# Kernel tuning notes

Hardware: AMD Instinct MI355X
Metric: run time of the kernel (lower is better)

## Reference

```python
import jax, jax.numpy as jnp
import numpy as np

L, H, DIN, T, B = 3, 512, 512, 256, 64


def _lstm_layer(x, m, h0, c0, Wih, Whh, b, reverse):
    # x: [T,B,Din], m: [T,B,1], h0/c0: [B,H], Wih: [4H,Din], Whh: [4H,H], b: [4H]
    def step(carry, xm):
        h, c = carry
        xt, mt = xm
        gates = xt @ Wih.T + h @ Whh.T + b  # [B,4H]
        i, f, g, o = jnp.split(gates, 4, axis=-1)
        c_n = (jax.nn.sigmoid(f) * c + jax.nn.sigmoid(i) * jnp.tanh(g)) * mt
        h_n = jax.nn.sigmoid(o) * jnp.tanh(c_n) * mt
        return (h_n, c_n), h_n
    (hT, cT), hs = jax.lax.scan(step, (h0, c0), (x, m), reverse=reverse)
    return hs, hT, cT


def setup_inputs():
    key = jax.random.key(0)
    ks = jax.random.split(key, 16)
    s = 0.05
    return {
        "x": jax.random.normal(ks[0], (T, B, DIN), jnp.float32),
        "masks": (jax.random.uniform(ks[1], (T, B, 1)) < 0.9).astype(jnp.float32),
        "f_Wih0": jax.random.normal(ks[2], (4 * H, DIN), jnp.float32) * s,
        "f_Wih_rest": jax.random.normal(ks[3], (L - 1, 4 * H, 2 * H), jnp.float32) * s,
        "f_Whh": jax.random.normal(ks[4], (L, 4 * H, H), jnp.float32) * s,
        "f_b": jnp.zeros((L, 4 * H), jnp.float32),
        "b_Wih0": jax.random.normal(ks[5], (4 * H, DIN), jnp.float32) * s,
        "b_Wih_rest": jax.random.normal(ks[6], (L - 1, 4 * H, 2 * H), jnp.float32) * s,
        "b_Whh": jax.random.normal(ks[7], (L, 4 * H, H), jnp.float32) * s,
        "b_b": jnp.zeros((L, 4 * H), jnp.float32),
        "f_init": jax.random.normal(ks[8], (L, 2, H), jnp.float32) * s,
        "b_init": jax.random.normal(ks[9], (L, 2, H), jnp.float32) * s,
        "proj_W": jax.random.normal(ks[10], (L - 1, 2 * H, 2 * H), jnp.float32) * s,
        "proj_b": jnp.zeros((L - 1, 2 * H), jnp.float32),
    }


def reference(x, masks, f_Wih0, f_Wih_rest, f_Whh, f_b, b_Wih0, b_Wih_rest, b_Whh, b_b,
              f_init, b_init, proj_W, proj_b):
    batch = x.shape[1]
    inp = x
    h_n, c_n = [], []
    for layer in range(L):
        Wih_f = f_Wih0 if layer == 0 else f_Wih_rest[layer - 1]
        Wih_b = b_Wih0 if layer == 0 else b_Wih_rest[layer - 1]
        h0f = jnp.broadcast_to(f_init[layer, 0], (batch, H))
        c0f = jnp.broadcast_to(f_init[layer, 1], (batch, H))
        h0b = jnp.broadcast_to(b_init[layer, 0], (batch, H))
        c0b = jnp.broadcast_to(b_init[layer, 1], (batch, H))
        fout, fh, fc = _lstm_layer(inp, masks, h0f, c0f, Wih_f, f_Whh[layer], f_b[layer], False)
        bout, bh, bc = _lstm_layer(inp, masks, h0b, c0b, Wih_b, b_Whh[layer], b_b[layer], True)
        h_n += [fh, bh]
        c_n += [fc, bc]
        out = jnp.concatenate([fout, bout], axis=-1)  # [T,B,2H]
        if layer > 0:
            g = jax.nn.sigmoid(out @ proj_W[layer - 1].T + proj_b[layer - 1])
            out = g * out + (1.0 - g) * inp
        inp = out
    return out, jnp.stack(h_n, 0), jnp.stack(c_n, 0)
```

## Files before the change

### kernel.cpp

```cpp
#include <hip/hip_runtime.h>

typedef __attribute__((ext_vector_type(8))) short short8;
typedef __attribute__((ext_vector_type(4))) float f32x4;

#define MFMA_B16(a, b, c) __builtin_amdgcn_mfma_f32_16x16x32_bf16((a), (b), (c), 0, 0, 0)

#define TSTEPS 256
#define NBATCH 64
#define HID    512
#define NBLK   32
#define UB     16
#define HSLOT  (NBATCH * HID)

__device__ __forceinline__ unsigned short f2bf(float f) {
  unsigned int u = __float_as_uint(f);
  u += 0x7fffu + ((u >> 16) & 1u);
  return (unsigned short)(u >> 16);
}
__device__ __forceinline__ float bf2f(unsigned short s) {
  return __uint_as_float(((unsigned int)s) << 16);
}
__device__ __forceinline__ float sigm(float x) { return 1.0f / (1.0f + __expf(-x)); }
__device__ __forceinline__ float tanhf_(float x) {
  float xc = fminf(fmaxf(x, -15.0f), 15.0f);
  float e = __expf(2.0f * xc);
  return (e - 1.0f) / (e + 1.0f);
}

__device__ __forceinline__ short8 ld_llc16(const unsigned short* p) {
  union { unsigned long long q[2]; short8 s; } u;
  unsigned long long* a = (unsigned long long*)p;
  u.q[0] = __hip_atomic_load(a,     __ATOMIC_RELAXED, __HIP_MEMORY_SCOPE_AGENT);
  u.q[1] = __hip_atomic_load(a + 1, __ATOMIC_RELAXED, __HIP_MEMORY_SCOPE_AGENT);
  return u.s;
}

__global__ void cvt_kernel(const float* __restrict__ src, unsigned short* __restrict__ dst, int n4) {
  int i = blockIdx.x * blockDim.x + threadIdx.x;
  int stride = gridDim.x * blockDim.x;
  for (; i < n4; i += stride) {
    f32x4 v = ((const f32x4*)src)[i];
    union { unsigned short u[4]; unsigned long long q; } o;
    o.u[0] = f2bf(v[0]); o.u[1] = f2bf(v[1]); o.u[2] = f2bf(v[2]); o.u[3] = f2bf(v[3]);
    ((unsigned long long*)dst)[i] = o.q;
  }
}

template<int K>
__global__ __launch_bounds__(256)
void gates_gemm(const unsigned short* __restrict__ act,
                const unsigned short* __restrict__ wcat,
                const float* __restrict__ bias_f,
                const float* __restrict__ bias_b,
                unsigned short* __restrict__ gates)
{
  const int lane = threadIdx.x & 63;
  const int wave = threadIdx.x >> 6;
  const int n = lane & 15, kb = lane >> 4;
  const int t0 = blockIdx.x * 2;
  const int rbase = blockIdx.y * 256 + wave * 64;

  f32x4 acc[2][4][4];
  #pragma unroll
  for (int mt = 0; mt < 4; ++mt) {
    f32x4 bi;
    #pragma unroll
    for (int i = 0; i < 4; ++i) {
      int r = rbase + mt * 16 + kb * 4 + i;
      bi[i] = (r < 2048) ? bias_f[r] : bias_b[r - 2048];
    }
    #pragma unroll
    for (int nt = 0; nt < 4; ++nt) { acc[0][mt][nt] = bi; acc[1][mt][nt] = bi; }
  }

  const unsigned short* wrow  = wcat + (size_t)(rbase + n) * K + kb * 8;
  const unsigned short* arow0 = act + ((size_t)t0 * 64 + n) * K + kb * 8;
  const unsigned short* arow1 = arow0 + (size_t)64 * K;
  #pragma unroll 2
  for (int ks = 0; ks < K / 32; ++ks) {
    short8 af[4], b0[4], b1[4];
    #pragma unroll
    for (int mt = 0; mt < 4; ++mt) af[mt] = *(const short8*)(wrow + (size_t)mt * 16 * K + ks * 32);
    #pragma unroll
    for (int nt = 0; nt < 4; ++nt) {
      b0[nt] = *(const short8*)(arow0 + (size_t)nt * 16 * K + ks * 32);
      b1[nt] = *(const short8*)(arow1 + (size_t)nt * 16 * K + ks * 32);
    }
    #pragma unroll
    for (int mt = 0; mt < 4; ++mt)
      #pragma unroll
      for (int nt = 0; nt < 4; ++nt) {
        acc[0][mt][nt] = MFMA_B16(af[mt], b0[nt], acc[0][mt][nt]);
        acc[1][mt][nt] = MFMA_B16(af[mt], b1[nt], acc[1][mt][nt]);
      }
  }

  #pragma unroll
  for (int t2 = 0; t2 < 2; ++t2) {
    unsigned short* gbase = gates + (size_t)(t0 + t2) * 4096 * 64;
    #pragma unroll
    for (int mt = 0; mt < 4; ++mt)
      #pragma unroll
      for (int i = 0; i < 4; ++i) {
        int r = rbase + mt * 16 + kb * 4 + i;
        #pragma unroll
        for (int nt = 0; nt < 4; ++nt)
          gbase[(size_t)r * 64 + nt * 16 + n] = f2bf(acc[t2][mt][nt][i]);
      }
  }
}

template<int DIN, int GXP>
__global__ __launch_bounds__(256, 1)
void scan_kernel(const unsigned short* __restrict__ act_in,
                 const unsigned short* __restrict__ gates,
                 unsigned short* __restrict__ act_out,
                 const unsigned short* __restrict__ wih_f,
                 const unsigned short* __restrict__ wih_b,
                 const unsigned short* __restrict__ whh_f,
                 const unsigned short* __restrict__ whh_b,
                 const float* __restrict__ bias_f,
                 const float* __restrict__ bias_b,
                 const float* __restrict__ init_f,
                 const float* __restrict__ init_b,
                 const float* __restrict__ masks,
                 unsigned short* hb,
                 unsigned int* bar,
                 float* out_h, float* out_c)
{
  const int bid  = blockIdx.x;
  const int dir  = bid >> 5;
  const int jb   = bid & (NBLK - 1);
  const int j0   = jb * UB;
  const int lane = threadIdx.x & 63;
  const int wave = threadIdx.x >> 6;
  const int n    = lane & 15;
  const int kb   = lane >> 4;
  const int u    = n & 7;
  const bool hif = (n >= 8);

  const unsigned short* wih = dir ? wih_b : wih_f;
  const unsigned short* whh = dir ? whh_b : whh_f;
  const float* bias = dir ? bias_b : bias_f;
  const float* init = dir ? init_b : init_f;
  const unsigned int* mypoll = bar + ((dir * 32 + jb) << 5) + (lane & 31);
  unsigned int* scat = bar + ((dir * 32 + (lane & 31)) << 5) + jb;
  unsigned short* hbd = hb + dir * (2 * HSLOT);
  float* oh = out_h + dir * (NBATCH * HID);
  float* oc = out_c + dir * (NBATCH * HID);

  int wr[4];
  wr[0] = hif ? (512 + j0 + u) : (j0 + u);
  wr[1] = wr[0] + 8;
  wr[2] = wr[0] + 1024;
  wr[3] = wr[0] + 1032;

  float bb[4];
  const unsigned short* wihp[4];
  #pragma unroll
  for (int q = 0; q < 4; ++q) {
    bb[q] = bias[wr[q]];
    wihp[q] = wih + (size_t)wr[q] * DIN + kb * 8;
  }

  __shared__ short8 wlds[16 * 4 * 64];
  __shared__ unsigned short lsm[NBATCH * UB];

  for (int g = threadIdx.x; g < 4096; g += 256) {
    int n_ = g & 15, kb_ = (g >> 4) & 3, q_ = (g >> 6) & 3, ks_ = g >> 8;
    int grow = ((n_ >= 8) ? 512 : 0) + j0 + (n_ & 7) + (q_ & 1) * 8 + (q_ >> 1) * 1024;
    wlds[g] = *(const short8*)(whh + (size_t)grow * HID + ks_ * 32 + kb_ * 8);
  }

  float cs[2][4];
  #pragma unroll
  for (int uh = 0; uh < 2; ++uh)
    #pragma unroll
    for (int i = 0; i < 4; ++i)
      cs[uh][i] = init[512 + j0 + uh * 8 + u];

  __syncthreads();

  if (wave == 0) {
    union { unsigned short us[16]; unsigned long long q[4]; } iv;
    #pragma unroll
    for (int k = 0; k < 16; ++k) iv.us[k] = f2bf(init[j0 + k]);
    unsigned long long* hd = (unsigned long long*)(hbd + jb * (NBATCH * UB) + lane * UB);
    #pragma unroll
    for (int k = 0; k < 4; ++k)
      __hip_atomic_store(hd + k, iv.q[k], __ATOMIC_RELAXED, __HIP_MEMORY_SCOPE_AGENT);
    asm volatile("s_waitcnt vmcnt(0)" ::: "memory");
    if (lane < 32)
      __hip_atomic_store(scat, 1u, __ATOMIC_RELAXED, __HIP_MEMORY_SCOPE_AGENT);
  }

  f32x4 acc_e[4], acc_o[4];

  auto wih_load = [&](int tstep) {
    #pragma unroll
    for (int q = 0; q < 4; ++q) {
      acc_e[q] = (f32x4){bb[q], bb[q], bb[q], bb[q]};
      acc_o[q] = (f32x4){0.f, 0.f, 0.f, 0.f};
    }
    const int tt2 = dir ? (TSTEPS - 1 - tstep) : tstep;
    const unsigned short* arow = act_in + ((size_t)tt2 * NBATCH + wave * 16 + n) * DIN + kb * 8;
    #pragma unroll
    for (int kt = 0; kt < DIN / 32; kt += 2) {
      short8 a0 = *(const short8*)(arow + kt * 32);
      short8 a1 = *(const short8*)(arow + kt * 32 + 32);
      #pragma unroll
      for (int q = 0; q < 4; ++q) {
        acc_e[q] = MFMA_B16(a0, *(const short8*)(wihp[q] + kt * 32), acc_e[q]);
        acc_o[q] = MFMA_B16(a1, *(const short8*)(wihp[q] + kt * 32 + 32), acc_o[q]);
      }
    }
  };

  if (!GXP) wih_load(0);

  for (int t = 0; t < TSTEPS; ++t) {
    const int tt = dir ? (TSTEPS - 1 - t) : t;

    f32x4 mk = *(const f32x4*)(masks + tt * NBATCH + wave * 16 + kb * 4);
    if (GXP) {
      const unsigned short* gb = gates + ((size_t)tt * 4096 + dir * 2048) * 64 + wave * 16 + kb * 4;
      #pragma unroll
      for (int q = 0; q < 4; ++q) {
        union { unsigned long long q8; unsigned short us[4]; } gv;
        gv.q8 = *(const unsigned long long*)(gb + (size_t)wr[q] * 64);
        acc_e[q] = (f32x4){bf2f(gv.us[0]), bf2f(gv.us[1]), bf2f(gv.us[2]), bf2f(gv.us[3])};
        acc_o[q] = (f32x4){0.f, 0.f, 0.f, 0.f};
      }
    }

    {
      const unsigned int tgt = t + 1;
      while (!__all((int)(__hip_atomic_load(mypoll, __ATOMIC_RELAXED, __HIP_MEMORY_SCOPE_AGENT) >= tgt)))
        __builtin_amdgcn_s_sleep(1);
    }

    {
      const unsigned short* hrow = hbd + (t & 1) * HSLOT
                                 + (kb >> 1) * 1024 + (kb & 1) * 8 + (wave * 16 + n) * UB;
      short8 hf[16];
      #pragma unroll
      for (int ks = 0; ks < 16; ++ks) hf[ks] = ld_llc16(hrow + ks * 2048);
      #pragma unroll
      for (int ks = 0; ks < 16; ++ks) {
        f32x4* ac = (ks & 1) ? acc_o : acc_e;
        #pragma unroll
        for (int q = 0; q < 4; ++q)
          ac[q] = MFMA_B16(hf[ks], wlds[(ks * 4 + q) * 64 + lane], ac[q]);
      }
    }

    #pragma unroll
    for (int uh = 0; uh < 2; ++uh) {
      f32x4 aif = acc_e[uh] + acc_o[uh];
      f32x4 ago = acc_e[2 + uh] + acc_o[2 + uh];
      f32x4 oif, ogo;
      #pragma unroll
      for (int r = 0; r < 4; ++r) {
        oif[r] = __shfl_xor(aif[r], 8, 64);
        ogo[r] = __shfl_xor(ago[r], 8, 64);
      }
      #pragma unroll
      for (int i = 0; i < 4; ++i) {
        float vi = hif ? oif[i] : aif[i];
        float vf = hif ? aif[i] : oif[i];
        float vg = hif ? ogo[i] : ago[i];
        float vo = hif ? ago[i] : ogo[i];
        float cn = (sigm(vf) * cs[uh][i] + sigm(vi) * tanhf_(vg)) * mk[i];
        float hvv = sigm(vo) * tanhf_(cn) * mk[i];
        cs[uh][i] = cn;
        if (!hif) {
          const int b = wave * 16 + kb * 4 + i;
          lsm[b * UB + uh * 8 + u] = f2bf(hvv);
          if (t == TSTEPS - 1) {
            oh[b * HID + j0 + uh * 8 + u] = hvv;
            oc[b * HID + j0 + uh * 8 + u] = cn;
          }
        }
      }
    }

    __syncthreads();

    if (wave == 0) {
      const unsigned long long* lq = (const unsigned long long*)lsm;
      unsigned long long q0 = lq[lane * 4 + 0];
      unsigned long long q1 = lq[lane * 4 + 1];
      unsigned long long q2 = lq[lane * 4 + 2];
      unsigned long long q3 = lq[lane * 4 + 3];
      if (t + 1 < TSTEPS) {
        unsigned short* hnxt = hbd + ((t + 1) & 1) * HSLOT;
        unsigned long long* hd = (unsigned long long*)(hnxt + jb * (NBATCH * UB) + lane * UB);
        __hip_atomic_store(hd + 0, q0, __ATOMIC_RELAXED, __HIP_MEMORY_SCOPE_AGENT);
        __hip_atomic_store(hd + 1, q1, __ATOMIC_RELAXED, __HIP_MEMORY_SCOPE_AGENT);
        __hip_atomic_store(hd + 2, q2, __ATOMIC_RELAXED, __HIP_MEMORY_SCOPE_AGENT);
        __hip_atomic_store(hd + 3, q3, __ATOMIC_RELAXED, __HIP_MEMORY_SCOPE_AGENT);
        asm volatile("s_waitcnt vmcnt(0)" ::: "memory");
        if (lane < 32)
          __hip_atomic_store(scat, (unsigned int)(t + 2), __ATOMIC_RELAXED, __HIP_MEMORY_SCOPE_AGENT);
      }
      union { unsigned long long q[2]; short8 s; } p0, p1;
      p0.q[0] = q0; p0.q[1] = q1; p1.q[0] = q2; p1.q[1] = q3;
      short8* ar = (short8*)(act_out + ((size_t)tt * NBATCH + lane) * (2 * HID) + dir * HID + j0);
      ar[0] = p0.s;
      ar[1] = p1.s;
    }

    if (!GXP && t + 1 < TSTEPS) wih_load(t + 1);
  }
}

template<int FINAL>
__global__ __launch_bounds__(256)
void highway_kernel(const unsigned short* __restrict__ raw,
                    unsigned short* __restrict__ inp,
                    const unsigned short* __restrict__ pw,
                    const float* __restrict__ pb,
                    float* __restrict__ outf)
{
  const int lane = threadIdx.x & 63;
  const int wave = threadIdx.x >> 6;
  const int n = lane & 15, kb = lane >> 4;
  const int r0 = blockIdx.x * 64 + wave * 16;
  const int c0 = blockIdx.y * 64;

  f32x4 acc[4];
  #pragma unroll
  for (int nt = 0; nt < 4; ++nt) {
    float b = pb[c0 + nt * 16 + n];
    acc[nt] = (f32x4){b, b, b, b};
  }
  const unsigned short* arow = raw + (r0 + n) * 1024 + kb * 8;
  #pragma unroll 4
  for (int kt = 0; kt < 32; ++kt) {
    short8 a = *(const short8*)(arow + kt * 32);
    #pragma unroll
    for (int nt = 0; nt < 4; ++nt) {
      short8 b = *(const short8*)(pw + (c0 + nt * 16 + n) * 1024 + kt * 32 + kb * 8);
      acc[nt] = MFMA_B16(a, b, acc[nt]);
    }
  }
  #pragma unroll
  for (int nt = 0; nt < 4; ++nt) {
    #pragma unroll
    for (int i = 0; i < 4; ++i) {
      int row = r0 + kb * 4 + i;
      int col = c0 + nt * 16 + n;
      float g = sigm(acc[nt][i]);
      float rv = bf2f(raw[row * 1024 + col]);
      float iv = bf2f(inp[row * 1024 + col]);
      float ov = g * rv + (1.0f - g) * iv;
      if (FINAL) outf[row * 1024 + col] = ov;
      else       inp[row * 1024 + col] = f2bf(ov);
    }
  }
}

extern "C" void kernel_launch(void* const* d_in, const int* in_sizes, int n_in,
                              void* d_out, int out_size, void* d_ws, size_t ws_size,
                              hipStream_t stream) {
  const float* x     = (const float*)d_in[0];
  const float* masks = (const float*)d_in[1];
  const float* fWih0 = (const float*)d_in[2];
  const float* fWihR = (const float*)d_in[3];
  const float* fWhh  = (const float*)d_in[4];
  const float* fb    = (const float*)d_in[5];
  const float* bWih0 = (const float*)d_in[6];
  const float* bWihR = (const float*)d_in[7];
  const float* bWhh  = (const float*)d_in[8];
  const float* bbias = (const float*)d_in[9];
  const float* fInit = (const float*)d_in[10];
  const float* bInit = (const float*)d_in[11];
  const float* projW = (const float*)d_in[12];
  const float* projB = (const float*)d_in[13];
  float* out = (float*)d_out;

  char* ws = (char*)d_ws;
  unsigned short* bufA  = (unsigned short*)(ws + 0);
  unsigned short* bufB  = (unsigned short*)(ws + 33554432);
  unsigned short* xbf   = (unsigned short*)(ws + 67108864);
  unsigned short* wcat0 = (unsigned short*)(ws + 83886080);
  unsigned short* wcat1 = (unsigned short*)(ws + 88080384);
  unsigned short* wcat2 = (unsigned short*)(ws + 96468992);
  unsigned short* whf   = (unsigned short*)(ws + 104857600);
  unsigned short* whb   = (unsigned short*)(ws + 111149056);
  unsigned short* pj    = (unsigned short*)(ws + 117440512);
  unsigned short* hbuf  = (unsigned short*)(ws + 121634816);
  unsigned int*   bar   = (unsigned int*)(ws + 121896960);
  unsigned short* gates = (unsigned short*)(ws + 121921536);
  const bool gx = ws_size >= 256139264ull;

  hipMemsetAsync(bar, 0, 24576, stream);

  cvt_kernel<<<1024, 256, 0, stream>>>(x,     xbf,   (256*64*512)  / 4);
  cvt_kernel<<<1024, 256, 0, stream>>>(fWih0, wcat0,              (2048*512)  / 4);
  cvt_kernel<<<1024, 256, 0, stream>>>(bWih0, wcat0 + 2048*512,   (2048*512)  / 4);
  cvt_kernel<<<1024, 256, 0, stream>>>(fWihR,             wcat1,             (2048*1024) / 4);
  cvt_kernel<<<1024, 256, 0, stream>>>(bWihR,             wcat1 + 2048*1024, (2048*1024) / 4);
  cvt_kernel<<<1024, 256, 0, stream>>>(fWihR + 2048*1024, wcat2,             (2048*1024) / 4);
  cvt_kernel<<<1024, 256, 0, stream>>>(bWihR + 2048*1024, wcat2 + 2048*1024, (2048*1024) / 4);
  cvt_kernel<<<1024, 256, 0, stream>>>(fWhh,  whf,   (3*2048*512)  / 4);
  cvt_kernel<<<1024, 256, 0, stream>>>(bWhh,  whb,   (3*2048*512)  / 4);
  cvt_kernel<<<1024, 256, 0, stream>>>(projW, pj,    (2*1024*1024) / 4);

  float* outH = out + 16777216;
  float* outC = out + 16777216 + 6*64*512;

  if (gx) {
    gates_gemm<512><<<dim3(128, 16), 256, 0, stream>>>(xbf, wcat0, fb, bbias, gates);
    scan_kernel<512, 1><<<64, 256, 0, stream>>>(
        xbf, gates, bufA,
        wcat0, wcat0 + 2048*512, whf, whb,
        fb, bbias, fInit, bInit, masks, hbuf, bar,
        outH, outC);
    gates_gemm<1024><<<dim3(128, 16), 256, 0, stream>>>(bufA, wcat1, fb + 2048, bbias + 2048, gates);
    scan_kernel<1024, 1><<<64, 256, 0, stream>>>(
        bufA, gates, bufB,
        wcat1, wcat1 + 2048*1024, whf + 2048*512, whb + 2048*512,
        fb + 2048, bbias + 2048, fInit + 1024, bInit + 1024, masks, hbuf, bar + 2048,
        outH + 2*64*512, outC + 2*64*512);
    highway_kernel<0><<<dim3(256, 16), 256, 0, stream>>>(bufB, bufA, pj, projB, nullptr);
    gates_gemm<1024><<<dim3(128, 16), 256, 0, stream>>>(bufA, wcat2, fb + 2*2048, bbias + 2*2048, gates);
    scan_kernel<1024, 1><<<64, 256, 0, stream>>>(
        bufA, gates, bufB,
        wcat2, wcat2 + 2048*1024, whf + 2*2048*512, whb + 2*2048*512,
        fb + 2*2048, bbias + 2*2048, fInit + 2048, bInit + 2048, masks, hbuf, bar + 4096,
        outH + 4*64*512, outC + 4*64*512);
    highway_kernel<1><<<dim3(256, 16), 256, 0, stream>>>(bufB, bufA, pj + 1024*1024, projB + 1024, out);
  } else {
    scan_kernel<512, 0><<<64, 256, 0, stream>>>(
        xbf, nullptr, bufA,
        wcat0, wcat0 + 2048*512, whf, whb,
        fb, bbias, fInit, bInit, masks, hbuf, bar,
        outH, outC);
    scan_kernel<1024, 0><<<64, 256, 0, stream>>>(
        bufA, nullptr, bufB,
        wcat1, wcat1 + 2048*1024, whf + 2048*512, whb + 2048*512,
        fb + 2048, bbias + 2048, fInit + 1024, bInit + 1024, masks, hbuf, bar + 2048,
        outH + 2*64*512, outC + 2*64*512);
    highway_kernel<0><<<dim3(256, 16), 256, 0, stream>>>(bufB, bufA, pj, projB, nullptr);
    scan_kernel<1024, 0><<<64, 256, 0, stream>>>(
        bufA, nullptr, bufB,
        wcat2, wcat2 + 2048*1024, whf + 2*2048*512, whb + 2*2048*512,
        fb + 2*2048, bbias + 2*2048, fInit + 2048, bInit + 2048, masks, hbuf, bar + 4096,
        outH + 4*64*512, outC + 4*64*512);
    highway_kernel<1><<<dim3(256, 16), 256, 0, stream>>>(bufB, bufA, pj + 1024*1024, projB + 1024, out);
  }
}
```

Baseline: 6.007 ms.

## Fuse recurrent scan with next-layer gates GEMM and highway via flag-driven worker blocks

Each layer's 64 recurrent scan blocks now share a persistent launch with 192 worker blocks. The workers claim tiles through an atomic counter and spin on per-timestep output flags, so the next layer's input-gate GEMM and the highway projection run while the scan is still producing timesteps. Work is handed out from the middle outward so the forward and backward directions can both finish a pair of timesteps early. The ten conversion kernels are merged into one launch. The cost is added flag polling, visibility concerns with the agent-scope relaxed atomics, possible competition between workers and the latency-critical scan blocks, and reliance on all 256 blocks being co-resident.

```diff
diff --git a/kernel.cpp b/kernel.cpp
--- a/kernel.cpp
+++ b/kernel.cpp
@@ -26,7 +26,17 @@
   float e = __expf(2.0f * xc);
   return (e - 1.0f) / (e + 1.0f);
 }
-
+__device__ __forceinline__ int moa(int k) { return (k & 1) ? (64 + (k >> 1)) : (63 - (k >> 1)); }
+
+__device__ __forceinline__ unsigned int ld_flag(const unsigned int* p) {
+  return __hip_atomic_load(p, __ATOMIC_RELAXED, __HIP_MEMORY_SCOPE_AGENT);
+}
+__device__ __forceinline__ void st_flag(unsigned int* p, unsigned int v) {
+  __hip_atomic_store(p, v, __ATOMIC_RELAXED, __HIP_MEMORY_SCOPE_AGENT);
+}
+__device__ __forceinline__ void st_u64(unsigned long long* p, unsigned long long v) {
+  __hip_atomic_store(p, v, __ATOMIC_RELAXED, __HIP_MEMORY_SCOPE_AGENT);
+}
 __device__ __forceinline__ short8 ld_llc16(const unsigned short* p) {
   union { unsigned long long q[2]; short8 s; } u;
   unsigned long long* a = (unsigned long long*)p;
@@ -34,12 +44,33 @@
   u.q[1] = __hip_atomic_load(a + 1, __ATOMIC_RELAXED, __HIP_MEMORY_SCOPE_AGENT);
   return u.s;
 }
-
-__global__ void cvt_kernel(const float* __restrict__ src, unsigned short* __restrict__ dst, int n4) {
-  int i = blockIdx.x * blockDim.x + threadIdx.x;
-  int stride = gridDim.x * blockDim.x;
-  for (; i < n4; i += stride) {
-    f32x4 v = ((const f32x4*)src)[i];
+__device__ __forceinline__ float ld_llc_bf16(const unsigned short* p) {
+  const unsigned int* p4 = (const unsigned int*)((unsigned long long)p & ~3ull);
+  unsigned int v = __hip_atomic_load(p4, __ATOMIC_RELAXED, __HIP_MEMORY_SCOPE_AGENT);
+  return bf2f(((unsigned long long)p & 2) ? (unsigned short)(v >> 16) : (unsigned short)v);
+}
+
+__global__ void cvt_all(const float* __restrict__ x,
+                        const float* __restrict__ fWih0, const float* __restrict__ bWih0,
+                        const float* __restrict__ fWihR, const float* __restrict__ bWihR,
+                        const float* __restrict__ fWhh,  const float* __restrict__ bWhh,
+                        const float* __restrict__ projW,
+                        unsigned short* __restrict__ dst)
+{
+  const int tot = 6815744;
+  for (int i = blockIdx.x * blockDim.x + threadIdx.x; i < tot; i += gridDim.x * blockDim.x) {
+    const float* src; int r;
+    if      (i < 2097152) { src = x;                 r = i; }
+    else if (i < 2359296) { src = fWih0;             r = i - 2097152; }
+    else if (i < 2621440) { src = bWih0;             r = i - 2359296; }
+    else if (i < 3145728) { src = fWihR;             r = i - 2621440; }
+    else if (i < 3670016) { src = bWihR;             r = i - 3145728; }
+    else if (i < 4194304) { src = fWihR + 2097152;   r = i - 3670016; }
+    else if (i < 4718592) { src = bWihR + 2097152;   r = i - 4194304; }
+    else if (i < 5505024) { src = fWhh;              r = i - 4718592; }
+    else if (i < 6291456) { src = bWhh;              r = i - 5505024; }
+    else                  { src = projW;             r = i - 6291456; }
+    f32x4 v = ((const f32x4*)src)[r];
     union { unsigned short u[4]; unsigned long long q; } o;
     o.u[0] = f2bf(v[0]); o.u[1] = f2bf(v[1]); o.u[2] = f2bf(v[2]); o.u[3] = f2bf(v[3]);
     ((unsigned long long*)dst)[i] = o.q;
@@ -72,7 +103,6 @@
     #pragma unroll
     for (int nt = 0; nt < 4; ++nt) { acc[0][mt][nt] = bi; acc[1][mt][nt] = bi; }
   }
-
   const unsigned short* wrow  = wcat + (size_t)(rbase + n) * K + kb * 8;
   const unsigned short* arow0 = act + ((size_t)t0 * 64 + n) * K + kb * 8;
   const unsigned short* arow1 = arow0 + (size_t)64 * K;
@@ -94,7 +124,6 @@
         acc[1][mt][nt] = MFMA_B16(af[mt], b1[nt], acc[1][mt][nt]);
       }
   }
-
   #pragma unroll
   for (int t2 = 0; t2 < 2; ++t2) {
     unsigned short* gbase = gates + (size_t)(t0 + t2) * 4096 * 64;
@@ -110,10 +139,331 @@
   }
 }
 
-template<int DIN, int GXP>
+template<int HMODE>
+__global__ __launch_bounds__(256, 1)
+void fused_kernel(const unsigned short* __restrict__ gates_in,
+                  unsigned short* __restrict__ act_out,
+                  const unsigned short* __restrict__ whh_f,
+                  const unsigned short* __restrict__ whh_b,
+                  const float* __restrict__ init_f,
+                  const float* __restrict__ init_b,
+                  const float* __restrict__ masks,
+                  unsigned short* hb,
+                  unsigned int* bar,
+                  float* out_h, float* out_c,
+                  const unsigned short* __restrict__ g_act,
+                  const unsigned short* __restrict__ g_wcat,
+                  const float* __restrict__ g_bf,
+                  const float* __restrict__ g_bb,
+                  unsigned short* __restrict__ g_out,
+                  unsigned short* __restrict__ hw_inp,
+                  const unsigned short* __restrict__ hw_pw,
+                  const float* __restrict__ hw_pb,
+                  float* __restrict__ hw_out)
+{
+  __shared__ short8 wlds[16 * 4 * 64 + 1536];
+  __shared__ unsigned short lsm[2][NBATCH * UB];
+  __shared__ int sh_w;
+
+  unsigned int* hflag_base  = bar;
+  unsigned int* aflag_base  = bar + 2048;
+  unsigned int* hwflag_base = bar + 6144;
+  unsigned int* claim       = bar + 10240;
+
+  const int lane = threadIdx.x & 63;
+  const int wave = threadIdx.x >> 6;
+  const int n    = lane & 15;
+  const int kb   = lane >> 4;
+
+  if (blockIdx.x < 64) {
+    const int bid = blockIdx.x;
+    const int dir = bid >> 5;
+    const int jb  = bid & (NBLK - 1);
+    const int j0  = jb * UB;
+    const int u   = n & 7;
+    const bool hif = (n >= 8);
+
+    const unsigned short* whh = dir ? whh_b : whh_f;
+    const float* init = dir ? init_b : init_f;
+    const unsigned int* mypoll = hflag_base + ((dir * 32 + jb) << 5) + (lane & 31);
+    unsigned int* scat = hflag_base + ((dir * 32 + (lane & 31)) << 5) + jb;
+    unsigned short* hbd = hb + dir * (2 * HSLOT);
+    float* oh = out_h + dir * (NBATCH * HID);
+    float* oc = out_c + dir * (NBATCH * HID);
+
+    int wr[4];
+    wr[0] = hif ? (512 + j0 + u) : (j0 + u);
+    wr[1] = wr[0] + 8;
+    wr[2] = wr[0] + 1024;
+    wr[3] = wr[0] + 1032;
+
+    for (int g = threadIdx.x; g < 4096; g += 256) {
+      int n_ = g & 15, kb_ = (g >> 4) & 3, q_ = (g >> 6) & 3, ks_ = g >> 8;
+      int grow = ((n_ >= 8) ? 512 : 0) + j0 + (n_ & 7) + (q_ & 1) * 8 + (q_ >> 1) * 1024;
+      wlds[g] = *(const short8*)(whh + (size_t)grow * HID + ks_ * 32 + kb_ * 8);
+    }
+
+    float cs[2][4];
+    #pragma unroll
+    for (int uh = 0; uh < 2; ++uh)
+      #pragma unroll
+      for (int i = 0; i < 4; ++i)
+        cs[uh][i] = init[512 + j0 + uh * 8 + u];
+
+    __syncthreads();
+
+    if (wave == 0) {
+      union { unsigned short us[16]; unsigned long long q[4]; } iv;
+      #pragma unroll
+      for (int k = 0; k < 16; ++k) iv.us[k] = f2bf(init[j0 + k]);
+      unsigned long long* hd = (unsigned long long*)(hbd + jb * (NBATCH * UB) + lane * UB);
+      #pragma unroll
+      for (int k = 0; k < 4; ++k) st_u64(hd + k, iv.q[k]);
+      asm volatile("s_waitcnt vmcnt(0)" ::: "memory");
+      if (lane < 32) st_flag(scat, 1u);
+    }
+
+    f32x4 acc_e[4], acc_o[4];
+
+    for (int t = 0; t < TSTEPS; ++t) {
+      const int tt = dir ? (TSTEPS - 1 - t) : t;
+
+      f32x4 mk = *(const f32x4*)(masks + tt * NBATCH + wave * 16 + kb * 4);
+      {
+        const unsigned short* gb = gates_in + ((size_t)tt * 4096 + dir * 2048) * 64 + wave * 16 + kb * 4;
+        #pragma unroll
+        for (int q = 0; q < 4; ++q) {
+          union { unsigned long long q8; unsigned short us[4]; } gv;
+          gv.q8 = *(const unsigned long long*)(gb + (size_t)wr[q] * 64);
+          acc_e[q] = (f32x4){bf2f(gv.us[0]), bf2f(gv.us[1]), bf2f(gv.us[2]), bf2f(gv.us[3])};
+          acc_o[q] = (f32x4){0.f, 0.f, 0.f, 0.f};
+        }
+      }
+
+      {
+        const unsigned int tgt = t + 1;
+        while (!__all((int)(ld_flag(mypoll) >= tgt)))
+          __builtin_amdgcn_s_sleep(1);
+      }
+
+      {
+        const unsigned short* hrow = hbd + (t & 1) * HSLOT
+                                   + (kb >> 1) * 1024 + (kb & 1) * 8 + (wave * 16 + n) * UB;
+        short8 hf[16];
+        #pragma unroll
+        for (int ks = 0; ks < 16; ++ks) hf[ks] = ld_llc16(hrow + ks * 2048);
+        #pragma unroll
+        for (int ks = 0; ks < 16; ++ks) {
+          f32x4* ac = (ks & 1) ? acc_o : acc_e;
+          #pragma unroll
+          for (int q = 0; q < 4; ++q)
+            ac[q] = MFMA_B16(hf[ks], wlds[(ks * 4 + q) * 64 + lane], ac[q]);
+        }
+      }
+
+      #pragma unroll
+      for (int uh = 0; uh < 2; ++uh) {
+        f32x4 aif = acc_e[uh] + acc_o[uh];
+        f32x4 ago = acc_e[2 + uh] + acc_o[2 + uh];
+        f32x4 oif, ogo;
+        #pragma unroll
+        for (int r = 0; r < 4; ++r) {
+          oif[r] = __shfl_xor(aif[r], 8, 64);
+          ogo[r] = __shfl_xor(ago[r], 8, 64);
+        }
+        #pragma unroll
+        for (int i = 0; i < 4; ++i) {
+          float vi = hif ? oif[i] : aif[i];
+          float vf = hif ? aif[i] : oif[i];
+          float vg = hif ? ogo[i] : ago[i];
+          float vo = hif ? ago[i] : ogo[i];
+          float cn = (sigm(vf) * cs[uh][i] + sigm(vi) * tanhf_(vg)) * mk[i];
+          float hvv = sigm(vo) * tanhf_(cn) * mk[i];
+          cs[uh][i] = cn;
+          if (!hif) {
+            const int b = wave * 16 + kb * 4 + i;
+            lsm[t & 1][b * UB + uh * 8 + u] = f2bf(hvv);
+            if (t == TSTEPS - 1) {
+              oh[b * HID + j0 + uh * 8 + u] = hvv;
+              oc[b * HID + j0 + uh * 8 + u] = cn;
+            }
+          }
+        }
+      }
+
+      __syncthreads();
+
+      if (wave == 0) {
+        if (t + 1 < TSTEPS) {
+          const unsigned long long* lq = (const unsigned long long*)lsm[t & 1];
+          unsigned long long q0 = lq[lane * 4 + 0];
+          unsigned long long q1 = lq[lane * 4 + 1];
+          unsigned long long q2 = lq[lane * 4 + 2];
+          unsigned long long q3 = lq[lane * 4 + 3];
+          unsigned long long* hd = (unsigned long long*)
+              (hbd + ((t + 1) & 1) * HSLOT + jb * (NBATCH * UB) + lane * UB);
+          st_u64(hd + 0, q0); st_u64(hd + 1, q1);
+          st_u64(hd + 2, q2); st_u64(hd + 3, q3);
+          asm volatile("s_waitcnt vmcnt(0)" ::: "memory");
+          if (lane < 32) st_flag(scat, (unsigned int)(t + 2));
+        }
+      } else if (wave == 1) {
+        const unsigned long long* lq = (const unsigned long long*)lsm[t & 1];
+        unsigned long long q0 = lq[lane * 4 + 0];
+        unsigned long long q1 = lq[lane * 4 + 1];
+        unsigned long long q2 = lq[lane * 4 + 2];
+        unsigned long long q3 = lq[lane * 4 + 3];
+        unsigned long long* ad = (unsigned long long*)
+            (act_out + ((size_t)tt * NBATCH + lane) * (2 * HID) + dir * HID + j0);
+        st_u64(ad + 0, q0); st_u64(ad + 1, q1);
+        st_u64(ad + 2, q2); st_u64(ad + 3, q3);
+        asm volatile("s_waitcnt vmcnt(0)" ::: "memory");
+        st_flag(aflag_base + ((dir * 64 + lane) << 5) + jb, (unsigned int)(t + 2));
+      }
+    }
+    return;
+  }
+
+  const int myline = blockIdx.x & 63;
+  const int NIT = (HMODE == 0) ? 2048 : (HMODE == 1) ? 2176 : 128;
+
+  for (;;) {
+    __syncthreads();
+    if (threadIdx.x == 0)
+      sh_w = (int)__hip_atomic_fetch_add(claim, 1u, __ATOMIC_RELAXED, __HIP_MEMORY_SCOPE_AGENT);
+    __syncthreads();
+    const int w = sh_w;
+    if (w >= NIT) return;
+
+    int a, kind, rb = 0;
+    if (HMODE == 0)      { a = moa(w >> 4); kind = 0; rb = w & 15; }
+    else if (HMODE == 1) { int tpk = w / 17, sub = w % 17; a = moa(tpk);
+                           kind = sub ? 0 : 1; rb = sub - 1; }
+    else                 { a = moa(w); kind = 2; }
+
+    if (HMODE == 1 && kind == 0) {
+      const unsigned int* hp = hwflag_base + a * 32;
+      while (ld_flag(hp) == 0) __builtin_amdgcn_s_sleep(8);
+    } else {
+      const unsigned int thr = (lane < 32) ? (unsigned int)(2 * a + 3)
+                                           : (unsigned int)(257 - 2 * a);
+      const unsigned int* fp = aflag_base + ((((lane < 32) ? 0 : 64) + myline) << 5) + (lane & 31);
+      while (!__all((int)(ld_flag(fp) >= thr))) __builtin_amdgcn_s_sleep(8);
+    }
+    __builtin_amdgcn_sched_barrier(0);
+
+    if (kind == 0) {
+      const int t0 = 2 * a;
+      const int rbase = rb * 256 + wave * 64;
+      f32x4 acc[2][4][4];
+      #pragma unroll
+      for (int mt = 0; mt < 4; ++mt) {
+        f32x4 bi;
+        #pragma unroll
+        for (int i = 0; i < 4; ++i) {
+          int r = rbase + mt * 16 + kb * 4 + i;
+          bi[i] = (r < 2048) ? g_bf[r] : g_bb[r - 2048];
+        }
+        #pragma unroll
+        for (int nt = 0; nt < 4; ++nt) { acc[0][mt][nt] = bi; acc[1][mt][nt] = bi; }
+      }
+      const unsigned short* wrow  = g_wcat + (size_t)(rbase + n) * 1024 + kb * 8;
+      const unsigned short* arow0 = g_act + ((size_t)t0 * 64 + n) * 1024 + kb * 8;
+      const unsigned short* arow1 = arow0 + (size_t)64 * 1024;
+      #pragma unroll 2
+      for (int ks = 0; ks < 32; ++ks) {
+        short8 af[4], b0[4], b1[4];
+        #pragma unroll
+        for (int mt = 0; mt < 4; ++mt) af[mt] = *(const short8*)(wrow + (size_t)mt * 16 * 1024 + ks * 32);
+        #pragma unroll
+        for (int nt = 0; nt < 4; ++nt) {
+          b0[nt] = ld_llc16(arow0 + (size_t)nt * 16 * 1024 + ks * 32);
+          b1[nt] = ld_llc16(arow1 + (size_t)nt * 16 * 1024 + ks * 32);
+        }
+        #pragma unroll
+        for (int mt = 0; mt < 4; ++mt)
+          #pragma unroll
+          for (int nt = 0; nt < 4; ++nt) {
+            acc[0][mt][nt] = MFMA_B16(af[mt], b0[nt], acc[0][mt][nt]);
+            acc[1][mt][nt] = MFMA_B16(af[mt], b1[nt], acc[1][mt][nt]);
+          }
+      }
+      #pragma unroll
+      for (int t2 = 0; t2 < 2; ++t2) {
+        unsigned short* gbase = g_out + (size_t)(t0 + t2) * 4096 * 64;
+        #pragma unroll
+        for (int mt = 0; mt < 4; ++mt)
+          #pragma unroll
+          for (int i = 0; i < 4; ++i) {
+            int r = rbase + mt * 16 + kb * 4 + i;
+            #pragma unroll
+            for (int nt = 0; nt < 4; ++nt)
+              gbase[(size_t)r * 64 + nt * 16 + n] = f2bf(acc[t2][mt][nt][i]);
+          }
+      }
+    } else {
+      unsigned short* hl = (unsigned short*)wlds + wave * 1024;
+      for (int rh = 0; rh < 2; ++rh) {
+        const int tt0 = 2 * a + rh;
+        const unsigned short* arow = act_out + ((size_t)tt0 * 64 + wave * 16 + n) * 1024 + kb * 8;
+        for (int ct = 0; ct < 16; ++ct) {
+          const int c0 = ct * 64;
+          f32x4 acc[4];
+          #pragma unroll
+          for (int nt = 0; nt < 4; ++nt) {
+            float b = hw_pb[c0 + nt * 16 + n];
+            acc[nt] = (f32x4){b, b, b, b};
+          }
+          #pragma unroll 4
+          for (int kt = 0; kt < 32; ++kt) {
+            short8 a8 = ld_llc16(arow + kt * 32);
+            #pragma unroll
+            for (int nt = 0; nt < 4; ++nt) {
+              short8 bw = *(const short8*)(hw_pw + (size_t)(c0 + nt * 16 + n) * 1024 + kt * 32 + kb * 8);
+              acc[nt] = MFMA_B16(a8, bw, acc[nt]);
+            }
+          }
+          #pragma unroll
+          for (int nt = 0; nt < 4; ++nt)
+            #pragma unroll
+            for (int i = 0; i < 4; ++i) {
+              const int rloc = kb * 4 + i;
+              const size_t R = (size_t)tt0 * 64 + wave * 16 + rloc;
+              const int col = c0 + nt * 16 + n;
+              float g = sigm(acc[nt][i]);
+              float rv = ld_llc_bf16(act_out + R * 1024 + col);
+              float ivv = bf2f(hw_inp[R * 1024 + col]);
+              float ov = g * rv + (1.0f - g) * ivv;
+              if (HMODE == 2) hw_out[R * 1024 + col] = ov;
+              else            hl[rloc * 64 + nt * 16 + n] = f2bf(ov);
+            }
+          if (HMODE == 1) {
+            asm volatile("s_waitcnt lgkmcnt(0)" ::: "memory");
+            const int r = lane >> 2, ch = lane & 3;
+            const unsigned long long* hq = (const unsigned long long*)hl;
+            unsigned long long v0 = hq[r * 16 + ch * 4 + 0];
+            unsigned long long v1 = hq[r * 16 + ch * 4 + 1];
+            unsigned long long v2 = hq[r * 16 + ch * 4 + 2];
+            unsigned long long v3 = hq[r * 16 + ch * 4 + 3];
+            unsigned long long* gd = (unsigned long long*)
+                (hw_inp + ((size_t)tt0 * 64 + wave * 16 + r) * 1024 + c0 + ch * 16);
+            st_u64(gd + 0, v0); st_u64(gd + 1, v1);
+            st_u64(gd + 2, v2); st_u64(gd + 3, v3);
+          }
+        }
+      }
+      if (HMODE == 1) {
+        asm volatile("s_waitcnt vmcnt(0)" ::: "memory");
+        __syncthreads();
+        if (threadIdx.x == 0) st_flag(hwflag_base + a * 32, 1u);
+      }
+    }
+  }
+}
+
+template<int DIN>
 __global__ __launch_bounds__(256, 1)
 void scan_kernel(const unsigned short* __restrict__ act_in,
-                 const unsigned short* __restrict__ gates,
                  unsigned short* __restrict__ act_out,
                  const unsigned short* __restrict__ wih_f,
                  const unsigned short* __restrict__ wih_b,
@@ -124,19 +474,16 @@
                  const float* __restrict__ init_f,
                  const float* __restrict__ init_b,
                  const float* __restrict__ masks,
-                 unsigned short* hb,
-                 unsigned int* bar,
+                 unsigned short* hb, unsigned int* bar,
                  float* out_h, float* out_c)
 {
-  const int bid  = blockIdx.x;
-  const int dir  = bid >> 5;
-  const int jb   = bid & (NBLK - 1);
-  const int j0   = jb * UB;
+  const int bid = blockIdx.x;
+  const int dir = bid >> 5;
+  const int jb = bid & (NBLK - 1);
+  const int j0 = jb * UB;
   const int lane = threadIdx.x & 63;
   const int wave = threadIdx.x >> 6;
-  const int n    = lane & 15;
-  const int kb   = lane >> 4;
-  const int u    = n & 7;
+  const int n = lane & 15, kb = lane >> 4, u = n & 7;
   const bool hif = (n >= 8);
 
   const unsigned short* wih = dir ? wih_b : wih_f;
@@ -151,10 +498,7 @@
 
   int wr[4];
   wr[0] = hif ? (512 + j0 + u) : (j0 + u);
-  wr[1] = wr[0] + 8;
-  wr[2] = wr[0] + 1024;
-  wr[3] = wr[0] + 1032;
-
+  wr[1] = wr[0] + 8; wr[2] = wr[0] + 1024; wr[3] = wr[0] + 1032;
   float bb[4];
   const unsigned short* wihp[4];
   #pragma unroll
@@ -162,40 +506,30 @@
     bb[q] = bias[wr[q]];
     wihp[q] = wih + (size_t)wr[q] * DIN + kb * 8;
   }
-
   __shared__ short8 wlds[16 * 4 * 64];
   __shared__ unsigned short lsm[NBATCH * UB];
-
   for (int g = threadIdx.x; g < 4096; g += 256) {
     int n_ = g & 15, kb_ = (g >> 4) & 3, q_ = (g >> 6) & 3, ks_ = g >> 8;
     int grow = ((n_ >= 8) ? 512 : 0) + j0 + (n_ & 7) + (q_ & 1) * 8 + (q_ >> 1) * 1024;
     wlds[g] = *(const short8*)(whh + (size_t)grow * HID + ks_ * 32 + kb_ * 8);
   }
-
   float cs[2][4];
   #pragma unroll
   for (int uh = 0; uh < 2; ++uh)
     #pragma unroll
-    for (int i = 0; i < 4; ++i)
-      cs[uh][i] = init[512 + j0 + uh * 8 + u];
-
+    for (int i = 0; i < 4; ++i) cs[uh][i] = init[512 + j0 + uh * 8 + u];
   __syncthreads();
-
   if (wave == 0) {
     union { unsigned short us[16]; unsigned long long q[4]; } iv;
     #pragma unroll
     for (int k = 0; k < 16; ++k) iv.us[k] = f2bf(init[j0 + k]);
     unsigned long long* hd = (unsigned long long*)(hbd + jb * (NBATCH * UB) + lane * UB);
     #pragma unroll
-    for (int k = 0; k < 4; ++k)
-      __hip_atomic_store(hd + k, iv.q[k], __ATOMIC_RELAXED, __HIP_MEMORY_SCOPE_AGENT);
+    for (int k = 0; k < 4; ++k) st_u64(hd + k, iv.q[k]);
     asm volatile("s_waitcnt vmcnt(0)" ::: "memory");
-    if (lane < 32)
-      __hip_atomic_store(scat, 1u, __ATOMIC_RELAXED, __HIP_MEMORY_SCOPE_AGENT);
-  }
-
+    if (lane < 32) st_flag(scat, 1u);
+  }
   f32x4 acc_e[4], acc_o[4];
-
   auto wih_load = [&](int tstep) {
     #pragma unroll
     for (int q = 0; q < 4; ++q) {
@@ -215,30 +549,14 @@
       }
     }
   };
-
-  if (!GXP) wih_load(0);
-
+  wih_load(0);
   for (int t = 0; t < TSTEPS; ++t) {
     const int tt = dir ? (TSTEPS - 1 - t) : t;
-
     f32x4 mk = *(const f32x4*)(masks + tt * NBATCH + wave * 16 + kb * 4);
-    if (GXP) {
-      const unsigned short* gb = gates + ((size_t)tt * 4096 + dir * 2048) * 64 + wave * 16 + kb * 4;
-      #pragma unroll
-      for (int q = 0; q < 4; ++q) {
-        union { unsigned long long q8; unsigned short us[4]; } gv;
-        gv.q8 = *(const unsigned long long*)(gb + (size_t)wr[q] * 64);
-        acc_e[q] = (f32x4){bf2f(gv.us[0]), bf2f(gv.us[1]), bf2f(gv.us[2]), bf2f(gv.us[3])};
-        acc_o[q] = (f32x4){0.f, 0.f, 0.f, 0.f};
-      }
-    }
-
     {
       const unsigned int tgt = t + 1;
-      while (!__all((int)(__hip_atomic_load(mypoll, __ATOMIC_RELAXED, __HIP_MEMORY_SCOPE_AGENT) >= tgt)))
-        __builtin_amdgcn_s_sleep(1);
-    }
-
+      while (!__all((int)(ld_flag(mypoll) >= tgt))) __builtin_amdgcn_s_sleep(1);
+    }
     {
       const unsigned short* hrow = hbd + (t & 1) * HSLOT
                                  + (kb >> 1) * 1024 + (kb & 1) * 8 + (wave * 16 + n) * UB;
@@ -253,7 +571,6 @@
           ac[q] = MFMA_B16(hf[ks], wlds[(ks * 4 + q) * 64 + lane], ac[q]);
       }
     }
-
     #pragma unroll
     for (int uh = 0; uh < 2; ++uh) {
       f32x4 aif = acc_e[uh] + acc_o[uh];
@@ -283,34 +600,25 @@
         }
       }
     }
-
     __syncthreads();
-
     if (wave == 0) {
       const unsigned long long* lq = (const unsigned long long*)lsm;
-      unsigned long long q0 = lq[lane * 4 + 0];
-      unsigned long long q1 = lq[lane * 4 + 1];
-      unsigned long long q2 = lq[lane * 4 + 2];
-      unsigned long long q3 = lq[lane * 4 + 3];
+      unsigned long long q0 = lq[lane * 4 + 0], q1 = lq[lane * 4 + 1];
+      unsigned long long q2 = lq[lane * 4 + 2], q3 = lq[lane * 4 + 3];
       if (t + 1 < TSTEPS) {
-        unsigned short* hnxt = hbd + ((t + 1) & 1) * HSLOT;
-        unsigned long long* hd = (unsigned long long*)(hnxt + jb * (NBATCH * UB) + lane * UB);
-        __hip_atomic_store(hd + 0, q0, __ATOMIC_RELAXED, __HIP_MEMORY_SCOPE_AGENT);
-        __hip_atomic_store(hd + 1, q1, __ATOMIC_RELAXED, __HIP_MEMORY_SCOPE_AGENT);
-        __hip_atomic_store(hd + 2, q2, __ATOMIC_RELAXED, __HIP_MEMORY_SCOPE_AGENT);
-        __hip_atomic_store(hd + 3, q3, __ATOMIC_RELAXED, __HIP_MEMORY_SCOPE_AGENT);
+        unsigned long long* hd = (unsigned long long*)
+            (hbd + ((t + 1) & 1) * HSLOT + jb * (NBATCH * UB) + lane * UB);
+        st_u64(hd + 0, q0); st_u64(hd + 1, q1);
+        st_u64(hd + 2, q2); st_u64(hd + 3, q3);
         asm volatile("s_waitcnt vmcnt(0)" ::: "memory");
-        if (lane < 32)
-          __hip_atomic_store(scat, (unsigned int)(t + 2), __ATOMIC_RELAXED, __HIP_MEMORY_SCOPE_AGENT);
+        if (lane < 32) st_flag(scat, (unsigned int)(t + 2));
       }
       union { unsigned long long q[2]; short8 s; } p0, p1;
       p0.q[0] = q0; p0.q[1] = q1; p1.q[0] = q2; p1.q[1] = q3;
       short8* ar = (short8*)(act_out + ((size_t)tt * NBATCH + lane) * (2 * HID) + dir * HID + j0);
-      ar[0] = p0.s;
-      ar[1] = p1.s;
-    }
-
-    if (!GXP && t + 1 < TSTEPS) wih_load(t + 1);
+      ar[0] = p0.s; ar[1] = p1.s;
+    }
+    if (t + 1 < TSTEPS) wih_load(t + 1);
   }
 }
 
@@ -327,7 +635,6 @@
   const int n = lane & 15, kb = lane >> 4;
   const int r0 = blockIdx.x * 64 + wave * 16;
   const int c0 = blockIdx.y * 64;
-
   f32x4 acc[4];
   #pragma unroll
   for (int nt = 0; nt < 4; ++nt) {
@@ -345,7 +652,7 @@
     }
   }
   #pragma unroll
-  for (int nt = 0; nt < 4; ++nt) {
+  for (int nt = 0; nt < 4; ++nt)
     #pragma unroll
     for (int i = 0; i < 4; ++i) {
       int row = r0 + kb * 4 + i;
@@ -357,7 +664,6 @@
       if (FINAL) outf[row * 1024 + col] = ov;
       else       inp[row * 1024 + col] = f2bf(ov);
     }
-  }
 }
 
 extern "C" void kernel_launch(void* const* d_in, const int* in_sizes, int n_in,
@@ -391,63 +697,47 @@
   unsigned short* pj    = (unsigned short*)(ws + 117440512);
   unsigned short* hbuf  = (unsigned short*)(ws + 121634816);
   unsigned int*   bar   = (unsigned int*)(ws + 121896960);
-  unsigned short* gates = (unsigned short*)(ws + 121921536);
-  const bool gx = ws_size >= 256139264ull;
-
-  hipMemsetAsync(bar, 0, 24576, stream);
-
-  cvt_kernel<<<1024, 256, 0, stream>>>(x,     xbf,   (256*64*512)  / 4);
-  cvt_kernel<<<1024, 256, 0, stream>>>(fWih0, wcat0,              (2048*512)  / 4);
-  cvt_kernel<<<1024, 256, 0, stream>>>(bWih0, wcat0 + 2048*512,   (2048*512)  / 4);
-  cvt_kernel<<<1024, 256, 0, stream>>>(fWihR,             wcat1,             (2048*1024) / 4);
-  cvt_kernel<<<1024, 256, 0, stream>>>(bWihR,             wcat1 + 2048*1024, (2048*1024) / 4);
-  cvt_kernel<<<1024, 256, 0, stream>>>(fWihR + 2048*1024, wcat2,             (2048*1024) / 4);
-  cvt_kernel<<<1024, 256, 0, stream>>>(bWihR + 2048*1024, wcat2 + 2048*1024, (2048*1024) / 4);
-  cvt_kernel<<<1024, 256, 0, stream>>>(fWhh,  whf,   (3*2048*512)  / 4);
-  cvt_kernel<<<1024, 256, 0, stream>>>(bWhh,  whb,   (3*2048*512)  / 4);
-  cvt_kernel<<<1024, 256, 0, stream>>>(projW, pj,    (2*1024*1024) / 4);
+  unsigned short* gates = (unsigned short*)(ws + 122093568);
+  const bool gx = ws_size >= 256311296ull;
+
+  hipMemsetAsync(bar, 0, 196608, stream);
+  cvt_all<<<1024, 256, 0, stream>>>(x, fWih0, bWih0, fWihR, bWihR, fWhh, bWhh, projW, xbf);
 
   float* outH = out + 16777216;
   float* outC = out + 16777216 + 6*64*512;
 
   if (gx) {
     gates_gemm<512><<<dim3(128, 16), 256, 0, stream>>>(xbf, wcat0, fb, bbias, gates);
-    scan_kernel<512, 1><<<64, 256, 0, stream>>>(
-        xbf, gates, bufA,
-        wcat0, wcat0 + 2048*512, whf, whb,
-        fb, bbias, fInit, bInit, masks, hbuf, bar,
-        outH, outC);
-    gates_gemm<1024><<<dim3(128, 16), 256, 0, stream>>>(bufA, wcat1, fb + 2048, bbias + 2048, gates);
-    scan_kernel<1024, 1><<<64, 256, 0, stream>>>(
-        bufA, gates, bufB,
-        wcat1, wcat1 + 2048*1024, whf + 2048*512, whb + 2048*512,
-        fb + 2048, bbias + 2048, fInit + 1024, bInit + 1024, masks, hbuf, bar + 2048,
+    fused_kernel<0><<<256, 256, 0, stream>>>(
+        gates, bufA, whf, whb, fInit, bInit, masks, hbuf, bar,
+        outH, outC,
+        bufA, wcat1, fb + 2048, bbias + 2048, gates,
+        bufA, pj, projB, out);
+    fused_kernel<1><<<256, 256, 0, stream>>>(
+        gates, bufB, whf + 2048*512, whb + 2048*512, fInit + 1024, bInit + 1024,
+        masks, hbuf, bar + 16384,
+        outH + 2*64*512, outC + 2*64*512,
+        bufA, wcat2, fb + 4096, bbias + 4096, gates,
+        bufA, pj, projB, out);
+    fused_kernel<2><<<256, 256, 0, stream>>>(
+        gates, bufB, whf + 2*2048*512, whb + 2*2048*512, fInit + 2048, bInit + 2048,
+        masks, hbuf, bar + 32768,
+        outH + 4*64*512, outC + 4*64*512,
+        bufA, wcat2, fb + 4096, bbias + 4096, gates,
+        bufA, pj + 1024*1024, projB + 1024, out);
+  } else {
+    scan_kernel<512><<<64, 256, 0, stream>>>(
+        xbf, bufA, wcat0, wcat0 + 2048*512, whf, whb,
+        fb, bbias, fInit, bInit, masks, hbuf, bar, outH, outC);
+    scan_kernel<1024><<<64, 256, 0, stream>>>(
+        bufA, bufB, wcat1, wcat1 + 2048*1024, whf + 2048*512, whb + 2048*512,
+        fb + 2048, bbias + 2048, fInit + 1024, bInit + 1024, masks, hbuf, bar + 16384,
         outH + 2*64*512, outC + 2*64*512);
     highway_kernel<0><<<dim3(256, 16), 256, 0, stream>>>(bufB, bufA, pj, projB, nullptr);
-    gates_gemm<1024><<<dim3(128, 16), 256, 0, stream>>>(bufA, wcat2, fb + 2*2048, bbias + 2*2048, gates);
-    scan_kernel<1024, 1><<<64, 256, 0, stream>>>(
-        bufA, gates, bufB,
-        wcat2, wcat2 + 2048*1024, whf + 2*2048*512, whb + 2*2048*512,
-        fb + 2*2048, bbias + 2*2048, fInit + 2048, bInit + 2048, masks, hbuf, bar + 4096,
+    scan_kernel<1024><<<64, 256, 0, stream>>>(
+        bufA, bufB, wcat2, wcat2 + 2048*1024, whf + 2*2048*512, whb + 2*2048*512,
+        fb + 4096, bbias + 4096, fInit + 2048, bInit + 2048, masks, hbuf, bar + 32768,
         outH + 4*64*512, outC + 4*64*512);
     highway_kernel<1><<<dim3(256, 16), 256, 0, stream>>>(bufB, bufA, pj + 1024*1024, projB + 1024, out);
-  } else {
-    scan_kernel<512, 0><<<64, 256, 0, stream>>>(
-        xbf, nullptr, bufA,
-        wcat0, wcat0 + 2048*512, whf, whb,
-        fb, bbias, fInit, bInit, masks, hbuf, bar,
-        outH, outC);
-    scan_kernel<1024, 0><<<64, 256, 0, stream>>>(
-        bufA, nullptr, bufB,
-        wcat1, wcat1 + 2048*1024, whf + 2048*512, whb + 2048*512,
-        fb + 2048, bbias + 2048, fInit + 1024, bInit + 1024, masks, hbuf, bar + 2048,
-        outH + 2*64*512, outC + 2*64*512);
-    highway_kernel<0><<<dim3(256, 16), 256, 0, stream>>>(bufB, bufA, pj, projB, nullptr);
-    scan_kernel<1024, 0><<<64, 256, 0, stream>>>(
-        bufA, nullptr, bufB,
-        wcat2, wcat2 + 2048*1024, whf + 2*2048*512, whb + 2*2048*512,
-        fb + 2*2048, bbias + 2*2048, fInit + 2048, bInit + 2048, masks, hbuf, bar + 4096,
-        outH + 4*64*512, outC + 4*64*512);
-    highway_kernel<1><<<dim3(256, 16), 256, 0, stream>>>(bufB, bufA, pj + 1024*1024, projB + 1024, out);
-  }
-}
+  }
+}
```

Result: slower. 16.37 ms (+172.6%).
